# Kernel optimization log

Measured on AMD Instinct MI355X. Metric: run time of the kernel, lower is better.

## Reference

```python
import jax, jax.numpy as jnp
import numpy as np

H = 128   # hidden_dim
E = 64    # embed_dim
M = 128   # max_num_nodes
B = 8
L = M * (M - 1) // 2  # 8128, lower-triangular vectorization length
THRESH = 20.0


def _pos_encoding(length, d):
    # sinusoidal encoding, base 10000 (PosEncoding module)
    pos = jnp.arange(length, dtype=jnp.float32)[:, None]
    div = jnp.exp(-jnp.log(10000.0) * jnp.arange(0, d, 2, dtype=jnp.float32) / d)
    ang = pos * div
    pe = jnp.zeros((length, d), dtype=jnp.float32)
    pe = pe.at[:, 0::2].set(jnp.sin(ang))
    pe = pe.at[:, 1::2].set(jnp.cos(ang))
    return pe


def _mlp(x, W1, b1, W2, b2):
    # BiGG-style MLP: Linear -> ReLU -> Linear
    return jax.nn.relu(x @ W1.T + b1) @ W2.T + b2


def _lstm_layer(x, W_ih, W_hh, h0, c0):
    # torch nn.LSTM single layer, bias=False, gate order i,f,g,o
    xW = jnp.einsum('bli,gi->lbg', x, W_ih)  # [L,B,4G]

    def step(carry, xt):
        h, c = carry
        gates = xt + h @ W_hh.T
        i, f, g, o = jnp.split(gates, 4, axis=-1)
        c = jax.nn.sigmoid(f) * c + jax.nn.sigmoid(i) * jnp.tanh(g)
        h = jax.nn.sigmoid(o) * jnp.tanh(c)
        return (h, c), h

    _, hs = jax.lax.scan(step, (h0, c0), xW)
    return jnp.transpose(hs, (1, 0, 2))  # [B,L,G]


def setup_inputs() -> dict:
    key = jax.random.key(0)
    ks = jax.random.split(key, 20)

    def g(k, shape, fan_in):
        return jax.random.normal(k, shape, dtype=jnp.float32) / np.sqrt(fan_in)

    # weighted lower-tri adjacency vector: w>0 on edges (p=0.1), 0 otherwise, no padding
    mask = (jax.random.uniform(ks[0], (B, L)) < 0.1).astype(jnp.float32)
    wts = 0.5 + 2.5 * jax.random.uniform(ks[1], (B, L))
    x_adj = (mask * wts).reshape(B, 1, L, 1)

    return {
        'x_adj': x_adj,
        'edge_exist_emb': g(ks[2], (2, 2 * E), 2 * E),
        'node_emb': g(ks[3], (M, E), E),
        'ew_W1': g(ks[4], (2 * E, 1), 1), 'ew_b1': jnp.zeros((2 * E,), jnp.float32),
        'ew_W2': g(ks[5], (E, 2 * E), 2 * E), 'ew_b2': jnp.zeros((E,), jnp.float32),
        'W_ih0': g(ks[6], (8 * H, 5 * E), 5 * E), 'W_hh0': g(ks[7], (8 * H, 2 * H), 2 * H),
        'W_ih1': g(ks[8], (8 * H, 2 * H), 2 * H), 'W_hh1': g(ks[9], (8 * H, 2 * H), 2 * H),
        'mu_W1': g(ks[10], (4 * H, 2 * H), 2 * H), 'mu_b1': jnp.zeros((4 * H,), jnp.float32),
        'mu_W2': g(ks[11], (1, 4 * H), 4 * H), 'mu_b2': jnp.zeros((1,), jnp.float32),
        'var_W1': g(ks[12], (4 * H, 2 * H), 2 * H), 'var_b1': jnp.zeros((4 * H,), jnp.float32),
        'var_W2': g(ks[13], (1, 4 * H), 4 * H), 'var_b2': jnp.zeros((1,), jnp.float32),
        'lg_W1': g(ks[14], (4 * H, 2 * H), 2 * H), 'lg_b1': jnp.zeros((4 * H,), jnp.float32),
        'lg_W2': g(ks[15], (1, 4 * H), 4 * H), 'lg_b2': jnp.zeros((1,), jnp.float32),
        'init_h': g(ks[16], (1, H), H), 'init_c': g(ks[17], (1, H), H),
    }


def reference(x_adj, edge_exist_emb, node_emb, ew_W1, ew_b1, ew_W2, ew_b2,
              W_ih0, W_hh0, W_ih1, W_hh1,
              mu_W1, mu_b1, mu_W2, mu_b2,
              var_W1, var_b1, var_W2, var_b2,
              lg_W1, lg_b1, lg_W2, lg_b2,
              init_h, init_c):
    x = x_adj.reshape(x_adj.shape[0], -1)  # squeeze(1) + last dim -> [B,L]
    b = x.shape[0]
    x_top = (x > 0).astype(jnp.float32)

    # teacher forcing: step t sees edge t-1 (start token = 0)
    prev_top = jnp.pad(x_top[:, :-1], ((0, 0), (1, 0)))
    prev_wt = jnp.pad(x[:, :-1], ((0, 0), (1, 0))) * prev_top

    ee = edge_exist_emb[prev_top.astype(jnp.int32)]                  # [B,L,2E]
    we = _mlp(prev_wt[..., None], ew_W1, ew_b1, ew_W2, ew_b2)        # [B,L,E]
    pe = _pos_encoding(L, E)                                         # [L,E]
    node_ids = np.repeat(np.arange(1, M), np.arange(1, M))           # row node of each lower-tri entry
    ne = node_emb[node_ids]                                          # [L,E]
    feat = jnp.concatenate([ee, we,
                            jnp.broadcast_to(pe, (b, L, E)),
                            jnp.broadcast_to(ne, (b, L, E))], axis=-1)  # [B,L,5E]

    h0 = jnp.tile(init_h, (b, 2))  # init state broadcast to 2H
    c0 = jnp.tile(init_c, (b, 2))
    out = _lstm_layer(feat, W_ih0, W_hh0, h0, c0)
    out = _lstm_layer(out, W_ih1, W_hh1, h0, c0)  # [B,L,2H]

    logits = _mlp(out, lg_W1, lg_b1, lg_W2, lg_b2)[..., 0]
    mus = _mlp(out, mu_W1, mu_b1, mu_W2, mu_b2)[..., 0]
    logv = _mlp(out, var_W1, var_b1, var_W2, var_b2)[..., 0]

    # reconstruction loss: BCE with logits, summed (no padding: constant_nodes)
    bce = jnp.maximum(logits, 0.0) - logits * x_top + jnp.log1p(jnp.exp(-jnp.abs(logits)))
    loss_r = jnp.sum(bce)

    # weight loss: Gaussian NLL on softminus(w), masked to true edges
    w_safe = jnp.where(x_top > 0, x, 1.0)
    sm = jnp.where(w_safe > THRESH, w_safe,
                   jnp.log(jnp.expm1(jnp.minimum(w_safe, THRESH))))
    loss_w = 0.5 * jnp.sum(x_top * (logv + jnp.square(mus - sm) * jnp.exp(-logv)))

    n = jnp.asarray(b * M, dtype=jnp.float32)  # sum(num_nodes)
    return loss_r / n, loss_w / n
```

## Files before the change

### kernel.cpp

```cpp
#include <hip/hip_runtime.h>

#define LSEQ 8128
#define NB 8
#define CORR_CAP 8192
#define HST 264
#define HROWS 9
#define HT1 (HROWS * HST)
#define RINGSZ 256
#define FLAG_R0A 0
#define FLAG_R0B 32
#define FLAG_R1A 64
#define FLAG_R1B 96
#define FLAG_H(q) (128 + (q) * 32)

typedef __attribute__((ext_vector_type(8))) short short8;
typedef __attribute__((ext_vector_type(4))) float float4e;
typedef unsigned long long ull;

#define MFMA16(a, b, c) __builtin_amdgcn_mfma_f32_16x16x32_bf16((a), (b), (c), 0, 0, 0)

#define WS_P      4096ul
#define WS_AEE    528384ul
#define WS_VPN    536576ul
#define WS_EIDX   17182720ul
#define WS_CORR   17444864ul
#define WS_URING  34222080ul
#define WS_HX     38416384ul
#define WS_H0     42610688ul
#define WS_H1     75907072ul

static __device__ __forceinline__ unsigned short f2bf(float f) {
  unsigned u = __float_as_uint(f);
  return (unsigned short)((u + 0x7fffu + ((u >> 16) & 1u)) >> 16);
}
static __device__ __forceinline__ float blo(unsigned u) { return __uint_as_float(u << 16); }
static __device__ __forceinline__ float bhi(unsigned u) { return __uint_as_float(u & 0xffff0000u); }
static __device__ __forceinline__ short8 pack8f(const float* __restrict__ p) {
  short8 r;
#pragma unroll
  for (int i = 0; i < 8; ++i) r[i] = (short)f2bf(p[i]);
  return r;
}
static __device__ __forceinline__ unsigned aload(const unsigned* p) {
  return __hip_atomic_load(p, __ATOMIC_RELAXED, __HIP_MEMORY_SCOPE_AGENT);
}
static __device__ __forceinline__ void astore(unsigned* p, unsigned v) {
  __hip_atomic_store(p, v, __ATOMIC_RELAXED, __HIP_MEMORY_SCOPE_AGENT);
}
static __device__ __forceinline__ ull aload64(const ull* p) {
  return __hip_atomic_load(p, __ATOMIC_RELAXED, __HIP_MEMORY_SCOPE_AGENT);
}
static __device__ __forceinline__ void astore64(ull* p, ull v) {
  __hip_atomic_store(p, v, __ATOMIC_RELAXED, __HIP_MEMORY_SCOPE_AGENT);
}
static __device__ __forceinline__ void fencev() {
  asm volatile("s_waitcnt vmcnt(0)" ::: "memory");
}
static __device__ __forceinline__ void drain8() {
  asm volatile("s_waitcnt vmcnt(8)" ::: "memory");
}
static __device__ __forceinline__ void cbar() { asm volatile("" ::: "memory"); }
static __device__ __forceinline__ void barrier_lgkm() {
  asm volatile("s_waitcnt lgkmcnt(0)\ns_barrier" ::: "memory");
}
static __device__ __forceinline__ float sigf(float x) { return 1.f / (1.f + __expf(-x)); }
static __device__ __forceinline__ float tanhf2(float x) { return 2.f / (1.f + __expf(-2.f * x)) - 1.f; }

__global__ void k_prep_P(const float* __restrict__ Wih0, const float* __restrict__ ewW2,
                         float* __restrict__ P) {
  int idx = blockIdx.x * 256 + threadIdx.x;
  int g = idx >> 7, k = idx & 127;
  const float* wr = Wih0 + (size_t)g * 320 + 128;
  float s = 0.f;
#pragma unroll 8
  for (int j = 0; j < 64; ++j) s += wr[j] * ewW2[j * 128 + k];
  P[idx] = s;
}

__global__ void k_prep_aee_init(const float* __restrict__ Wih0, const float* __restrict__ ee,
                                const float* __restrict__ b1, const float* __restrict__ b2,
                                const float* __restrict__ P, const float* __restrict__ inith,
                                float* __restrict__ aee, unsigned short* __restrict__ h0u,
                                unsigned short* __restrict__ h1u) {
  int idx = blockIdx.x * 256 + threadIdx.x;
  int s = idx >> 10, g = idx & 1023;
  const float* wr = Wih0 + (size_t)g * 320;
  float a = 0.f;
#pragma unroll 8
  for (int i = 0; i < 128; ++i) a += wr[i] * ee[s * 128 + i];
#pragma unroll 8
  for (int j = 0; j < 64; ++j) a += wr[128 + j] * b2[j];
  const float* pr = P + (size_t)g * 128;
#pragma unroll 8
  for (int k = 0; k < 128; ++k) a += pr[k] * fmaxf(b1[k], 0.f);
  aee[s * 1024 + g] = a;
  unsigned short hv = f2bf(inith[idx & 127]);
  h0u[idx] = hv;
  h1u[idx] = hv;
}

__global__ void k_prep_vpn(const float* __restrict__ Wih0, const float* __restrict__ nemb,
                           const float* __restrict__ aee, unsigned short* __restrict__ vpn) {
  __shared__ float pn[128];
  int t = blockIdx.x, tid = threadIdx.x;
  if (tid < 32) {
    float div = expf(-9.2103403719761836f * (float)(2 * tid) / 64.f);
    float ang = (float)t * div;
    pn[2 * tid] = sinf(ang);
    pn[2 * tid + 1] = cosf(ang);
  } else if (tid < 96) {
    int r = (int)((1.f + sqrtf(8.f * (float)t + 1.f)) * 0.5f);
    while (r * (r + 1) / 2 <= t) ++r;
    while (r * (r - 1) / 2 > t) --r;
    pn[64 + (tid - 32)] = nemb[r * 64 + (tid - 32)];
  }
  __syncthreads();
#pragma unroll
  for (int rr = 0; rr < 4; ++rr) {
    int row = rr * 256 + tid;
    const float* wr = Wih0 + (size_t)row * 320 + 192;
    float s = 0.f;
#pragma unroll 8
    for (int i = 0; i < 128; ++i) s += wr[i] * pn[i];
    vpn[(size_t)t * 1024 + row] = f2bf(s + aee[row]);
  }
}

__global__ void k_prep_eidx(const float* __restrict__ xadj, int* __restrict__ eidx,
                            unsigned* __restrict__ counter) {
  int idx = blockIdx.x * 256 + threadIdx.x;
  if (idx >= NB * LSEQ) return;
  int t = idx % LSEQ;
  int e = -1;
  if (t > 0 && xadj[idx - 1] > 0.f) {
    e = (int)atomicAdd(counter, 1u);
    if (e >= CORR_CAP) e = -1;
  }
  eidx[idx] = e;
}

__global__ void k_prep_corr(const float* __restrict__ xadj, const float* __restrict__ w1,
                            const float* __restrict__ b1, const float* __restrict__ P,
                            const float* __restrict__ aee, const int* __restrict__ eidx,
                            unsigned short* __restrict__ corr) {
  __shared__ float rh[128];
  int bid = blockIdx.x;
  int e = eidx[bid];
  if (e < 0) return;
  int tid = threadIdx.x;
  float wt = xadj[bid - 1];
  if (tid < 128) {
    float bb = b1[tid];
    rh[tid] = fmaxf(wt * w1[tid] + bb, 0.f) - fmaxf(bb, 0.f);
  }
  __syncthreads();
#pragma unroll
  for (int rr = 0; rr < 4; ++rr) {
    int row = rr * 256 + tid;
    const float* pr = P + (size_t)row * 128;
    float s = 0.f;
#pragma unroll 8
    for (int k = 0; k < 128; ++k) s += pr[k] * rh[k];
    corr[(size_t)e * 1024 + row] = f2bf(s + aee[1024 + row] - aee[row]);
  }
}

template <int LAYER, int H>
static __device__ __forceinline__ void recur(
    const float* __restrict__ Wrec, const unsigned short* __restrict__ vpn,
    const int* __restrict__ eidx, const unsigned short* __restrict__ corr,
    const unsigned* __restrict__ uring, const float* __restrict__ inith,
    const float* __restrict__ initc, unsigned* flags, unsigned* hout,
    ull* hx, unsigned short* hT, int tid, int myflag) {
  const int wv = tid >> 6, l = tid & 63, lm = l & 15, lk = l >> 4;
  const int lmr = (lm < 8) ? lm : 8;
  const int base = H * 128;
  const int rbase = 128 - base;
  const int bb = lm & 7;
  const int hi = (lm >> 3) & 1;
  const int jg = base + wv * 16 + lk * 4;
  const int jo = jg + hi * 2;
  unsigned budget = 100000000u;

  ull* hx_my = hx + (size_t)((LAYER * 2 + H) * 4) * 512;
  const ull* hx_rm = hx + (size_t)((LAYER * 2 + (1 - H)) * 4) * 512;
  const int widx = bb * 64 + wv * 8 + lk * 2 + hi;
  const int fb = tid >> 6, fl = tid & 63;
  const int rmc = fb * 64 + fl;
  const int fj = rbase + fl * 2;

  for (int i = tid; i < HT1; i += 512) hT[i] = 0;
  __syncthreads();
  {
    int b = tid >> 6, j0i = (tid & 63) * 4;
    unsigned h01 = (unsigned)f2bf(inith[j0i & 127]) | ((unsigned)f2bf(inith[(j0i + 1) & 127]) << 16);
    unsigned h23 = (unsigned)f2bf(inith[(j0i + 2) & 127]) | ((unsigned)f2bf(inith[(j0i + 3) & 127]) << 16);
    *(uint2*)&hT[b * HST + j0i] = make_uint2(h01, h23);
  }
  float cc[2];
  cc[0] = initc[jo & 127];
  cc[1] = initc[(jo + 1) & 127];

  short8 wf[4][8];
#pragma unroll
  for (int g = 0; g < 4; ++g) {
    int row = g * 256 + base + wv * 16 + lm;
#pragma unroll
    for (int ks = 0; ks < 8; ++ks)
      wf[g][ks] = pack8f(Wrec + (size_t)row * 256 + ks * 32 + lk * 8);
  }
  __syncthreads();

  int e_nxt = (LAYER == 0) ? eidx[bb * LSEQ] : -1;
  unsigned Tm = 0;

  for (int t = 0; t < LSEQ; ++t) {
    unsigned vvs[4], cvs[4];
#pragma unroll
    for (int g = 0; g < 4; ++g) { vvs[g] = 0u; cvs[g] = 0u; }
    if (LAYER == 0) {
      const unsigned short* vp = vpn + (size_t)t * 1024;
#pragma unroll
      for (int g = 0; g < 4; ++g) vvs[g] = *(const unsigned*)(vp + g * 256 + jo);
      int e = e_nxt;
      if (t + 1 < LSEQ) e_nxt = eidx[bb * LSEQ + t + 1];
      if (e >= 0) {
        const unsigned short* cp = corr + (size_t)e * 1024;
#pragma unroll
        for (int g = 0; g < 4; ++g) cvs[g] = *(const unsigned*)(cp + g * 256 + jo);
      }
    }

    float4e acc[4];
#pragma unroll
    for (int g = 0; g < 4; ++g) acc[g] = (float4e){0.f, 0.f, 0.f, 0.f};
    __builtin_amdgcn_s_setprio(1);
#pragma unroll
    for (int ksl = 0; ksl < 4; ++ksl) {
      const int ks = H * 4 + ksl;
      short8 hb = *(const short8*)(hT + lmr * HST + ks * 32 + lk * 8);
#pragma unroll
      for (int g = 0; g < 4; ++g) acc[g] = MFMA16(wf[g][ks], hb, acc[g]);
    }
    __builtin_amdgcn_s_setprio(0);

    if (LAYER == 1) {
      while (Tm < (unsigned)(t + 1)) {
        unsigned c0 = aload(flags + FLAG_H(0)), c1 = aload(flags + FLAG_H(1));
        unsigned c2 = aload(flags + FLAG_H(2)), c3 = aload(flags + FLAG_H(3));
        unsigned m0 = c0 < c1 ? c0 : c1, m1 = c2 < c3 ? c2 : c3;
        Tm = m0 < m1 ? m0 : m1;
        if (--budget == 0) break;
        asm volatile("s_sleep 1");
      }
      cbar();
      const unsigned* ub = uring + (size_t)(t & (RINGSZ - 1)) * 4096 + bb * 512;
#pragma unroll
      for (int g = 0; g < 4; ++g) vvs[g] = aload(ub + ((g * 256 + jo) >> 1));
    }

    if (t > 0) {
      ull q;
      do {
        q = aload64(hx_rm + (size_t)(t & 3) * 512 + rmc);
      } while ((unsigned)(q >> 32) != (unsigned)t && --budget);
      cbar();
      *(unsigned*)&hT[fb * HST + fj] = (unsigned)q;
    }
    barrier_lgkm();

    __builtin_amdgcn_s_setprio(1);
#pragma unroll
    for (int ksl = 0; ksl < 4; ++ksl) {
      const int ks = (4 - H * 4) + ksl;
      short8 hb = *(const short8*)(hT + lmr * HST + ks * 32 + lk * 8);
#pragma unroll
      for (int g = 0; g < 4; ++g) acc[g] = MFMA16(wf[g][ks], hb, acc[g]);
    }
    __builtin_amdgcn_s_setprio(0);

    float g0[4], g1[4];
#pragma unroll
    for (int g = 0; g < 4; ++g) {
      float s2 = __shfl_xor(acc[g][2], 8);
      float s3 = __shfl_xor(acc[g][3], 8);
      float a0 = hi ? s2 : acc[g][0];
      float a1 = hi ? s3 : acc[g][1];
      g0[g] = a0 + blo(vvs[g]) + (LAYER == 0 ? blo(cvs[g]) : 0.f);
      g1[g] = a1 + bhi(vvs[g]) + (LAYER == 0 ? bhi(cvs[g]) : 0.f);
    }
    {
      float cn0 = sigf(g0[1]) * cc[0] + sigf(g0[0]) * tanhf2(g0[2]);
      float cn1 = sigf(g1[1]) * cc[1] + sigf(g1[0]) * tanhf2(g1[2]);
      cc[0] = cn0;
      cc[1] = cn1;
      float hv0 = sigf(g0[3]) * tanhf2(cn0);
      float hv1 = sigf(g1[3]) * tanhf2(cn1);
      unsigned hp = (unsigned)f2bf(hv0) | ((unsigned)f2bf(hv1) << 16);
      *(unsigned*)&hT[bb * HST + jo] = hp;
      astore(hout + (size_t)(t + 1) * 1024 + bb * 128 + (jo >> 1), hp);
      astore64(hx_my + (size_t)((t + 1) & 3) * 512 + widx,
               (ull)hp | (((ull)(unsigned)(t + 1)) << 32));
    }

    if (LAYER == 0) {
      if ((t & 3) == 3) {
        if (t == LSEQ - 1) fencev(); else drain8();
      }
      barrier_lgkm();
      if ((t & 3) == 3 && tid == 0)
        astore(flags + myflag, (t == LSEQ - 1) ? (unsigned)LSEQ : (unsigned)t);
    } else {
      barrier_lgkm();
      if ((t & 63) == 63 && tid == 0) astore(flags + myflag, (unsigned)t);
    }
  }
}

static __device__ __forceinline__ void uprod(
    int q, const float* __restrict__ Wih1, unsigned* flags,
    const unsigned* __restrict__ h0w, unsigned* uring, unsigned short* hB, int tid) {
  const int wv = tid >> 6, l = tid & 63, lm = l & 15, lk = l >> 4;
  const int lmr = (lm < 8) ? lm : 8;
  unsigned budget = 100000000u;
  for (int i = tid; i < 2 * HT1; i += 512) hB[i] = 0;
  short8 wf[2][8];
#pragma unroll
  for (int tt = 0; tt < 2; ++tt) {
    int row = q * 256 + (wv * 2 + tt) * 16 + lm;
#pragma unroll
    for (int ks = 0; ks < 8; ++ks)
      wf[tt][ks] = pack8f(Wih1 + (size_t)row * 256 + ks * 32 + lk * 8);
  }
  __syncthreads();
  unsigned FcA = 0, FcB = 0, Fm = 0, PcA = 0, PcB = 0, Pm = 0;
  while (Fm < 2u) {
    FcA = aload(flags + FLAG_R0A);
    FcB = aload(flags + FLAG_R0B);
    Fm = FcA < FcB ? FcA : FcB;
    if (--budget == 0) break;
    asm volatile("s_sleep 1");
  }
  cbar();
  {
    uint2 t0 = ((const uint2*)(h0w + (size_t)1 * 1024))[tid];
    *(uint2*)((unsigned*)hB + wv * (HST / 2) + l * 2) = t0;
  }
  uint2 hw = ((const uint2*)(h0w + (size_t)2 * 1024))[tid];
  barrier_lgkm();
  for (int t = 0; t < LSEQ; ++t) {
    const int rdo = (t & 1) * HT1;
    const int wro = ((t + 1) & 1) * HT1;
    if (t + 1 < LSEQ)
      *(uint2*)((unsigned*)(hB + wro) + wv * (HST / 2) + l * 2) = hw;
    short8 bfr[8];
#pragma unroll
    for (int ks = 0; ks < 8; ++ks)
      bfr[ks] = *(const short8*)(hB + rdo + lmr * HST + ks * 32 + lk * 8);
    float4e a0 = {0.f, 0.f, 0.f, 0.f}, a1 = a0;
    __builtin_amdgcn_s_setprio(1);
#pragma unroll
    for (int ks = 0; ks < 8; ++ks) {
      a0 = MFMA16(wf[0][ks], bfr[ks], a0);
      a1 = MFMA16(wf[1][ks], bfr[ks], a1);
    }
    __builtin_amdgcn_s_setprio(0);
    int slot = t & (RINGSZ - 1);
    if (lm < 8) {
#pragma unroll
      for (int tt = 0; tt < 2; ++tt) {
        float4e a = tt ? a1 : a0;
        int g0 = q * 256 + (wv * 2 + tt) * 16 + lk * 4;
        unsigned p0 = (unsigned)f2bf(a[0]) | ((unsigned)f2bf(a[1]) << 16);
        unsigned p1 = (unsigned)f2bf(a[2]) | ((unsigned)f2bf(a[3]) << 16);
        unsigned* up = uring + (size_t)slot * 4096 + lm * 512 + (g0 >> 1);
        astore(up, p0);
        astore(up + 1, p1);
      }
    }
    if (t + 2 < LSEQ) {
      while (Fm < (unsigned)(t + 3)) {
        FcA = aload(flags + FLAG_R0A);
        FcB = aload(flags + FLAG_R0B);
        Fm = FcA < FcB ? FcA : FcB;
        if (--budget == 0) break;
        asm volatile("s_sleep 1");
      }
      while ((unsigned)(t + 1) >= Pm + 192u) {
        PcA = aload(flags + FLAG_R1A);
        PcB = aload(flags + FLAG_R1B);
        Pm = PcA < PcB ? PcA : PcB;
        if (--budget == 0) break;
        asm volatile("s_sleep 1");
      }
      cbar();
      hw = ((const uint2*)(h0w + (size_t)(t + 3) * 1024))[tid];
    }
    if ((t & 7) == 7) {
      if (t == LSEQ - 1) fencev(); else drain8();
      barrier_lgkm();
      if (tid == 0)
        astore(flags + FLAG_H(q), (t == LSEQ - 1) ? (unsigned)LSEQ : (unsigned)(t - 1));
    } else {
      barrier_lgkm();
    }
  }
}

__global__ __launch_bounds__(512, 2) void k_lstm(
    const float* __restrict__ Whh0, const float* __restrict__ Wih1,
    const float* __restrict__ Whh1, const unsigned short* __restrict__ vpn,
    const int* __restrict__ eidx, const unsigned short* __restrict__ corr,
    const float* __restrict__ inith, const float* __restrict__ initc,
    unsigned* flags, unsigned* uring, ull* hx, unsigned* h0w, unsigned* h1w) {
  __shared__ __align__(16) unsigned short hT[2 * HT1];
  const int tid = threadIdx.x;
  const int bx = blockIdx.x;
  if (bx == 0)
    recur<0, 0>(Whh0, vpn, eidx, corr, nullptr, inith, initc, flags, h0w, hx, hT, tid, FLAG_R0A);
  else if (bx == 1)
    recur<0, 1>(Whh0, vpn, eidx, corr, nullptr, inith, initc, flags, h0w, hx, hT, tid, FLAG_R0B);
  else if (bx == 2)
    recur<1, 0>(Whh1, nullptr, nullptr, nullptr, uring, inith, initc, flags, h1w, hx, hT, tid, FLAG_R1A);
  else if (bx == 3)
    recur<1, 1>(Whh1, nullptr, nullptr, nullptr, uring, inith, initc, flags, h1w, hx, hT, tid, FLAG_R1B);
  else
    uprod(bx - 4, Wih1, flags, h0w, uring, hT, tid);
}

__global__ __launch_bounds__(256, 2) void k_heads(
    const unsigned short* __restrict__ h1u, const float* __restrict__ xadj,
    const float* __restrict__ lgW1, const float* __restrict__ lgb1,
    const float* __restrict__ lgW2, const float* __restrict__ lgb2,
    const float* __restrict__ muW1, const float* __restrict__ mub1,
    const float* __restrict__ muW2, const float* __restrict__ mub2,
    const float* __restrict__ vaW1, const float* __restrict__ vab1,
    const float* __restrict__ vaW2, const float* __restrict__ vab2,
    float* dout) {
  __shared__ float vals[4][3][64];
  const int tid = threadIdx.x;
  const int v = tid >> 6, l = tid & 63, lm = l & 15, lk = l >> 4;
  const int wid = blockIdx.x * 4 + v;
  const int m0 = wid * 64;

  short8 afr[4][8];
#pragma unroll
  for (int tt = 0; tt < 4; ++tt)
#pragma unroll
    for (int ks = 0; ks < 8; ++ks)
      afr[tt][ks] = *(const short8*)(h1u + (size_t)(m0 + tt * 16 + lm) * 256 + 2048 + ks * 32 + lk * 8);

  const float* W1s[3] = {lgW1, muW1, vaW1};
  const float* b1s[3] = {lgb1, mub1, vab1};
  const float* W2s[3] = {lgW2, muW2, vaW2};

  for (int h = 0; h < 3; ++h) {
    float accr[4][4];
#pragma unroll
    for (int tt = 0; tt < 4; ++tt)
#pragma unroll
      for (int r = 0; r < 4; ++r) accr[tt][r] = 0.f;
    const float* W1p = W1s[h];
    const float* b1p = b1s[h];
    const float* W2p = W2s[h];
    for (int nt = 0; nt < 32; ++nt) {
      float4e c0 = {0.f, 0.f, 0.f, 0.f}, c1 = c0, c2 = c0, c3 = c0;
      const float* wp = W1p + (size_t)(nt * 16 + lm) * 256;
#pragma unroll
      for (int ks = 0; ks < 8; ++ks) {
        short8 bfr = pack8f(wp + ks * 32 + lk * 8);
        c0 = MFMA16(afr[0][ks], bfr, c0);
        c1 = MFMA16(afr[1][ks], bfr, c1);
        c2 = MFMA16(afr[2][ks], bfr, c2);
        c3 = MFMA16(afr[3][ks], bfr, c3);
      }
      float bias = b1p[nt * 16 + lm], w2v = W2p[nt * 16 + lm];
#pragma unroll
      for (int r = 0; r < 4; ++r) {
        accr[0][r] += fmaxf(c0[r] + bias, 0.f) * w2v;
        accr[1][r] += fmaxf(c1[r] + bias, 0.f) * w2v;
        accr[2][r] += fmaxf(c2[r] + bias, 0.f) * w2v;
        accr[3][r] += fmaxf(c3[r] + bias, 0.f) * w2v;
      }
    }
#pragma unroll
    for (int tt = 0; tt < 4; ++tt)
#pragma unroll
      for (int r = 0; r < 4; ++r) {
        float a2 = accr[tt][r];
        a2 += __shfl_xor(a2, 1);
        a2 += __shfl_xor(a2, 2);
        a2 += __shfl_xor(a2, 4);
        a2 += __shfl_xor(a2, 8);
        if (lm == 0) vals[v][h][tt * 16 + lk * 4 + r] = a2;
      }
  }
  __syncthreads();
  {
    int m = m0 + l;
    int tq = m >> 3, b = m & 7;
    float z = vals[v][0][l] + lgb2[0];
    float mu = vals[v][1][l] + mub2[0];
    float lv = vals[v][2][l] + vab2[0];
    float x = xadj[(size_t)b * LSEQ + tq];
    float xt = (x > 0.f) ? 1.f : 0.f;
    float lr = fmaxf(z, 0.f) - z * xt + log1pf(expf(-fabsf(z)));
    float lw = 0.f;
    if (x > 0.f) {
      float sm = (x > 20.f) ? x : logf(expm1f(fminf(x, 20.f)));
      float d = mu - sm;
      lw = 0.5f * (lv + d * d * expf(-lv));
    }
#pragma unroll
    for (int d2 = 1; d2 < 64; d2 <<= 1) {
      lr += __shfl_xor(lr, d2);
      lw += __shfl_xor(lw, d2);
    }
    if (l == 0) {
      atomicAdd(dout + 0, lr * (1.f / 1024.f));
      atomicAdd(dout + 1, lw * (1.f / 1024.f));
    }
  }
}

extern "C" void kernel_launch(void* const* d_in, const int* in_sizes, int n_in,
                              void* d_out, int out_size, void* d_ws, size_t ws_size,
                              hipStream_t stream) {
  const float* x_adj = (const float*)d_in[0];
  const float* ee    = (const float*)d_in[1];
  const float* nemb  = (const float*)d_in[2];
  const float* ewW1  = (const float*)d_in[3];
  const float* ewb1  = (const float*)d_in[4];
  const float* ewW2  = (const float*)d_in[5];
  const float* ewb2  = (const float*)d_in[6];
  const float* Wih0  = (const float*)d_in[7];
  const float* Whh0  = (const float*)d_in[8];
  const float* Wih1  = (const float*)d_in[9];
  const float* Whh1  = (const float*)d_in[10];
  const float* muW1  = (const float*)d_in[11];
  const float* mub1  = (const float*)d_in[12];
  const float* muW2  = (const float*)d_in[13];
  const float* mub2  = (const float*)d_in[14];
  const float* vaW1  = (const float*)d_in[15];
  const float* vab1  = (const float*)d_in[16];
  const float* vaW2  = (const float*)d_in[17];
  const float* vab2  = (const float*)d_in[18];
  const float* lgW1  = (const float*)d_in[19];
  const float* lgb1  = (const float*)d_in[20];
  const float* lgW2  = (const float*)d_in[21];
  const float* lgb2  = (const float*)d_in[22];
  const float* inith = (const float*)d_in[23];
  const float* initc = (const float*)d_in[24];

  char* wsb = (char*)d_ws;
  unsigned* flags      = (unsigned*)wsb;
  unsigned* counter    = (unsigned*)(wsb + 2048);
  float* P             = (float*)(wsb + WS_P);
  float* aee           = (float*)(wsb + WS_AEE);
  unsigned short* vpn  = (unsigned short*)(wsb + WS_VPN);
  int* eidx            = (int*)(wsb + WS_EIDX);
  unsigned short* corr = (unsigned short*)(wsb + WS_CORR);
  unsigned* uring      = (unsigned*)(wsb + WS_URING);
  ull* hx              = (ull*)(wsb + WS_HX);
  unsigned* h0w        = (unsigned*)(wsb + WS_H0);
  unsigned* h1w        = (unsigned*)(wsb + WS_H1);
  unsigned short* h0u  = (unsigned short*)(wsb + WS_H0);
  unsigned short* h1u  = (unsigned short*)(wsb + WS_H1);

  (void)in_sizes; (void)n_in; (void)ws_size;

  hipMemsetAsync(d_ws, 0, 4096, stream);
  hipMemsetAsync(wsb + WS_HX, 0, 65536, stream);
  hipMemsetAsync(d_out, 0, (size_t)out_size * 4, stream);

  k_prep_P<<<512, 256, 0, stream>>>(Wih0, ewW2, P);
  k_prep_aee_init<<<8, 256, 0, stream>>>(Wih0, ee, ewb1, ewb2, P, inith, aee, h0u, h1u);
  k_prep_vpn<<<LSEQ, 256, 0, stream>>>(Wih0, nemb, aee, vpn);
  k_prep_eidx<<<(NB * LSEQ) / 256, 256, 0, stream>>>(x_adj, eidx, counter);
  k_prep_corr<<<NB * LSEQ, 256, 0, stream>>>(x_adj, ewW1, ewb1, P, aee, eidx, corr);
  k_lstm<<<8, 512, 0, stream>>>(Whh0, Wih1, Whh1, vpn, eidx, corr, inith, initc,
                                flags, uring, hx, h0w, h1w);
  k_heads<<<254, 256, 0, stream>>>(h1u, x_adj, lgW1, lgb1, lgW2, lgb2,
                                   muW1, mub1, muW2, mub2, vaW1, vab1, vaW2, vab2,
                                   (float*)d_out);
}
```

Baseline: 18.94 ms.

## Per-wave remote hidden-state fetch with double-buffered local state and split block placement

Each wave now fetches the partner block's full hidden-state half into its own private LDS region, polling eight 64-bit tagged slots per lane. This removes the block-wide barrier that previously sat between the remote-state exchange and the second MFMA half. The local hidden half is double-buffered by timestep parity, so writes for step t+1 do not race with reads of step t. The grid grows to 16 blocks so the paired recurrence blocks land at indices 0/8 and 1/9, presumably on different dies or XCDs. The spin budget is also lowered; the risks are redundant global polling traffic per wave and placement assumptions about block scheduling.

Result: slower. 27.71 ms (+46.4%).

```diff
diff --git a/kernel.cpp b/kernel.cpp
--- a/kernel.cpp
+++ b/kernel.cpp
@@ -6,6 +6,10 @@
 #define HST 264
 #define HROWS 9
 #define HT1 (HROWS * HST)
+#define HSTL 136
+#define HTL (9 * HSTL)
+#define RWR 68
+#define RWW (9 * RWR)
 #define RINGSZ 256
 #define FLAG_R0A 0
 #define FLAG_R0B 32
@@ -171,7 +175,7 @@
     const int* __restrict__ eidx, const unsigned short* __restrict__ corr,
     const unsigned* __restrict__ uring, const float* __restrict__ inith,
     const float* __restrict__ initc, unsigned* flags, unsigned* hout,
-    ull* hx, unsigned short* hT, int tid, int myflag) {
+    ull* hx, unsigned short* hT, unsigned* rws, int tid, int myflag) {
   const int wv = tid >> 6, l = tid & 63, lm = l & 15, lk = l >> 4;
   const int lmr = (lm < 8) ? lm : 8;
   const int base = H * 128;
@@ -180,22 +184,34 @@
   const int hi = (lm >> 3) & 1;
   const int jg = base + wv * 16 + lk * 4;
   const int jo = jg + hi * 2;
-  unsigned budget = 100000000u;
+  const int jl = jo - base;
+  unsigned budget = 20000000u;
 
   ull* hx_my = hx + (size_t)((LAYER * 2 + H) * 4) * 512;
   const ull* hx_rm = hx + (size_t)((LAYER * 2 + (1 - H)) * 4) * 512;
   const int widx = bb * 64 + wv * 8 + lk * 2 + hi;
-  const int fb = tid >> 6, fl = tid & 63;
-  const int rmc = fb * 64 + fl;
-  const int fj = rbase + fl * 2;
-
-  for (int i = tid; i < HT1; i += 512) hT[i] = 0;
+
+  unsigned* rw = rws + wv * RWW;
+  const int sb = l >> 3;
+  const int sj = (l & 7) * 8;
+
+  for (int i = tid; i < 2 * HTL; i += 512) hT[i] = 0;
   __syncthreads();
   {
-    int b = tid >> 6, j0i = (tid & 63) * 4;
-    unsigned h01 = (unsigned)f2bf(inith[j0i & 127]) | ((unsigned)f2bf(inith[(j0i + 1) & 127]) << 16);
-    unsigned h23 = (unsigned)f2bf(inith[(j0i + 2) & 127]) | ((unsigned)f2bf(inith[(j0i + 3) & 127]) << 16);
-    *(uint2*)&hT[b * HST + j0i] = make_uint2(h01, h23);
+    int b = tid >> 6, c0 = (tid & 63) * 2;
+    unsigned hv = (unsigned)f2bf(inith[(base + c0) & 127]) |
+                  ((unsigned)f2bf(inith[(base + c0 + 1) & 127]) << 16);
+    *(unsigned*)&hT[HTL + b * HSTL + c0] = hv;
+  }
+  for (int i = l; i < RWW; i += 64) {
+    int row = i / RWR, jp = i % RWR;
+    unsigned v = 0u;
+    if (row < 8 && jp < 64) {
+      int c = jp * 2;
+      v = (unsigned)f2bf(inith[(rbase + c) & 127]) |
+          ((unsigned)f2bf(inith[(rbase + c + 1) & 127]) << 16);
+    }
+    rw[i] = v;
   }
   float cc[2];
   cc[0] = initc[jo & 127];
@@ -215,6 +231,14 @@
   unsigned Tm = 0;
 
   for (int t = 0; t < LSEQ; ++t) {
+    const int rd = ((t + 1) & 1) * HTL;
+    const int wr = (t & 1) * HTL;
+    ull q[8];
+    const ull* ps = hx_rm + (size_t)(t & 3) * 512 + l * 8;
+    if (t > 0) {
+#pragma unroll
+      for (int i = 0; i < 8; ++i) q[i] = aload64(ps + i);
+    }
     unsigned vvs[4], cvs[4];
 #pragma unroll
     for (int g = 0; g < 4; ++g) { vvs[g] = 0u; cvs[g] = 0u; }
@@ -237,10 +261,9 @@
     __builtin_amdgcn_s_setprio(1);
 #pragma unroll
     for (int ksl = 0; ksl < 4; ++ksl) {
-      const int ks = H * 4 + ksl;
-      short8 hb = *(const short8*)(hT + lmr * HST + ks * 32 + lk * 8);
-#pragma unroll
-      for (int g = 0; g < 4; ++g) acc[g] = MFMA16(wf[g][ks], hb, acc[g]);
+      short8 hb = *(const short8*)(hT + rd + lmr * HSTL + ksl * 32 + lk * 8);
+#pragma unroll
+      for (int g = 0; g < 4; ++g) acc[g] = MFMA16(wf[g][H * 4 + ksl], hb, acc[g]);
     }
     __builtin_amdgcn_s_setprio(0);
 
@@ -260,36 +283,43 @@
     }
 
     if (t > 0) {
-      ull q;
-      do {
-        q = aload64(hx_rm + (size_t)(t & 3) * 512 + rmc);
-      } while ((unsigned)(q >> 32) != (unsigned)t && --budget);
+      const unsigned tg = (unsigned)t;
+      for (;;) {
+        bool ok = true;
+#pragma unroll
+        for (int i = 0; i < 8; ++i) ok &= ((unsigned)(q[i] >> 32) == tg);
+        if (ok || --budget == 0) break;
+#pragma unroll
+        for (int i = 0; i < 8; ++i) q[i] = aload64(ps + i);
+      }
       cbar();
-      *(unsigned*)&hT[fb * HST + fj] = (unsigned)q;
-    }
-    barrier_lgkm();
+      uint4 w0, w1;
+      w0.x = (unsigned)q[0]; w0.y = (unsigned)q[1]; w0.z = (unsigned)q[2]; w0.w = (unsigned)q[3];
+      w1.x = (unsigned)q[4]; w1.y = (unsigned)q[5]; w1.z = (unsigned)q[6]; w1.w = (unsigned)q[7];
+      *(uint4*)&rw[sb * RWR + sj] = w0;
+      *(uint4*)&rw[sb * RWR + sj + 4] = w1;
+    }
 
     __builtin_amdgcn_s_setprio(1);
 #pragma unroll
     for (int ksl = 0; ksl < 4; ++ksl) {
-      const int ks = (4 - H * 4) + ksl;
-      short8 hb = *(const short8*)(hT + lmr * HST + ks * 32 + lk * 8);
-#pragma unroll
-      for (int g = 0; g < 4; ++g) acc[g] = MFMA16(wf[g][ks], hb, acc[g]);
+      short8 hb = *(const short8*)(rw + lmr * RWR + ksl * 16 + lk * 4);
+#pragma unroll
+      for (int g = 0; g < 4; ++g) acc[g] = MFMA16(wf[g][(4 - H * 4) + ksl], hb, acc[g]);
     }
     __builtin_amdgcn_s_setprio(0);
 
-    float g0[4], g1[4];
-#pragma unroll
-    for (int g = 0; g < 4; ++g) {
-      float s2 = __shfl_xor(acc[g][2], 8);
-      float s3 = __shfl_xor(acc[g][3], 8);
-      float a0 = hi ? s2 : acc[g][0];
-      float a1 = hi ? s3 : acc[g][1];
-      g0[g] = a0 + blo(vvs[g]) + (LAYER == 0 ? blo(cvs[g]) : 0.f);
-      g1[g] = a1 + bhi(vvs[g]) + (LAYER == 0 ? bhi(cvs[g]) : 0.f);
-    }
     {
+      float g0[4], g1[4];
+#pragma unroll
+      for (int g = 0; g < 4; ++g) {
+        float s2 = __shfl_xor(acc[g][2], 8);
+        float s3 = __shfl_xor(acc[g][3], 8);
+        float a0 = hi ? s2 : acc[g][0];
+        float a1 = hi ? s3 : acc[g][1];
+        g0[g] = a0 + blo(vvs[g]) + (LAYER == 0 ? blo(cvs[g]) : 0.f);
+        g1[g] = a1 + bhi(vvs[g]) + (LAYER == 0 ? bhi(cvs[g]) : 0.f);
+      }
       float cn0 = sigf(g0[1]) * cc[0] + sigf(g0[0]) * tanhf2(g0[2]);
       float cn1 = sigf(g1[1]) * cc[1] + sigf(g1[0]) * tanhf2(g1[2]);
       cc[0] = cn0;
@@ -297,10 +327,10 @@
       float hv0 = sigf(g0[3]) * tanhf2(cn0);
       float hv1 = sigf(g1[3]) * tanhf2(cn1);
       unsigned hp = (unsigned)f2bf(hv0) | ((unsigned)f2bf(hv1) << 16);
-      *(unsigned*)&hT[bb * HST + jo] = hp;
-      astore(hout + (size_t)(t + 1) * 1024 + bb * 128 + (jo >> 1), hp);
       astore64(hx_my + (size_t)((t + 1) & 3) * 512 + widx,
                (ull)hp | (((ull)(unsigned)(t + 1)) << 32));
+      *(unsigned*)&hT[wr + bb * HSTL + jl] = hp;
+      astore(hout + (size_t)(t + 1) * 1024 + bb * 128 + (jo >> 1), hp);
     }
 
     if (LAYER == 0) {
@@ -322,7 +352,7 @@
     const unsigned* __restrict__ h0w, unsigned* uring, unsigned short* hB, int tid) {
   const int wv = tid >> 6, l = tid & 63, lm = l & 15, lk = l >> 4;
   const int lmr = (lm < 8) ? lm : 8;
-  unsigned budget = 100000000u;
+  unsigned budget = 20000000u;
   for (int i = tid; i < 2 * HT1; i += 512) hB[i] = 0;
   short8 wf[2][8];
 #pragma unroll
@@ -413,19 +443,21 @@
     const int* __restrict__ eidx, const unsigned short* __restrict__ corr,
     const float* __restrict__ inith, const float* __restrict__ initc,
     unsigned* flags, unsigned* uring, ull* hx, unsigned* h0w, unsigned* h1w) {
-  __shared__ __align__(16) unsigned short hT[2 * HT1];
+  __shared__ __align__(16) unsigned smem[6120];
   const int tid = threadIdx.x;
   const int bx = blockIdx.x;
+  unsigned short* hT = (unsigned short*)smem;
+  unsigned* rws = smem + (2 * HTL) / 2;
   if (bx == 0)
-    recur<0, 0>(Whh0, vpn, eidx, corr, nullptr, inith, initc, flags, h0w, hx, hT, tid, FLAG_R0A);
+    recur<0, 0>(Whh0, vpn, eidx, corr, nullptr, inith, initc, flags, h0w, hx, hT, rws, tid, FLAG_R0A);
+  else if (bx == 8)
+    recur<0, 1>(Whh0, vpn, eidx, corr, nullptr, inith, initc, flags, h0w, hx, hT, rws, tid, FLAG_R0B);
   else if (bx == 1)
-    recur<0, 1>(Whh0, vpn, eidx, corr, nullptr, inith, initc, flags, h0w, hx, hT, tid, FLAG_R0B);
-  else if (bx == 2)
-    recur<1, 0>(Whh1, nullptr, nullptr, nullptr, uring, inith, initc, flags, h1w, hx, hT, tid, FLAG_R1A);
-  else if (bx == 3)
-    recur<1, 1>(Whh1, nullptr, nullptr, nullptr, uring, inith, initc, flags, h1w, hx, hT, tid, FLAG_R1B);
-  else
-    uprod(bx - 4, Wih1, flags, h0w, uring, hT, tid);
+    recur<1, 0>(Whh1, nullptr, nullptr, nullptr, uring, inith, initc, flags, h1w, hx, hT, rws, tid, FLAG_R1A);
+  else if (bx == 9)
+    recur<1, 1>(Whh1, nullptr, nullptr, nullptr, uring, inith, initc, flags, h1w, hx, hT, rws, tid, FLAG_R1B);
+  else if (bx >= 2 && bx <= 5)
+    uprod(bx - 2, Wih1, flags, h0w, uring, (unsigned short*)smem, tid);
 }
 
 __global__ __launch_bounds__(256, 2) void k_heads(
@@ -578,8 +610,8 @@
   k_prep_vpn<<<LSEQ, 256, 0, stream>>>(Wih0, nemb, aee, vpn);
   k_prep_eidx<<<(NB * LSEQ) / 256, 256, 0, stream>>>(x_adj, eidx, counter);
   k_prep_corr<<<NB * LSEQ, 256, 0, stream>>>(x_adj, ewW1, ewb1, P, aee, eidx, corr);
-  k_lstm<<<8, 512, 0, stream>>>(Whh0, Wih1, Whh1, vpn, eidx, corr, inith, initc,
-                                flags, uring, hx, h0w, h1w);
+  k_lstm<<<16, 512, 0, stream>>>(Whh0, Wih1, Whh1, vpn, eidx, corr, inith, initc,
+                                 flags, uring, hx, h0w, h1w);
   k_heads<<<254, 256, 0, stream>>>(h1u, x_adj, lgW1, lgb1, lgW2, lgb2,
                                    muW1, mub1, muW2, mub2, vaW1, vab1, vaW2, vab2,
                                    (float*)d_out);
```
